# Kernel optimization log

Measured on AMD Instinct MI355X. Metric: run time of the kernel, lower is better.

Reference implementation:

```python
import jax, jax.numpy as jnp
import numpy as np

BITS = 4
GROUP = 128
MAXQ = 2 ** BITS - 1  # 15 for asymmetric 4-bit


def round_ste(x):
    # straight-through rounding: round in fwd, identity in bwd
    return x + jax.lax.stop_gradient(jnp.round(x) - x)


def quant_weight(weight, v, min_scale, max_scale):
    """Groupwise asymmetric fake-quant (quantize + dequantize) of weight.

    weight: [O, I], v: [O, I] learnable rounding offsets,
    min_scale/max_scale: [O*I/GROUP] learnable min/max scales in [-1, 0].
    """
    O, I = weight.shape
    w = weight.reshape(-1, GROUP)          # [G, GROUP]
    vv = v.reshape(-1, GROUP)              # [G, GROUP]
    wmin_t = jnp.minimum(w.min(axis=1), 0.0)  # [G]
    wmax_t = jnp.maximum(w.max(axis=1), 0.0)  # [G]
    # forward clamps min/max scale into [-1, 0] before use
    wmin = wmin_t * (jnp.clip(min_scale, -1.0, 0.0) + 1.0)
    wmax = wmax_t * (jnp.clip(max_scale, -1.0, 0.0) + 1.0)
    degenerate = (wmin == 0.0) & (wmax == 0.0)
    wmin = jnp.where(degenerate, -1.0, wmin)
    wmax = jnp.where(degenerate, 1.0, wmax)
    # scale stored at fp16 precision (scale_dtype), then used in fp32 math
    scale = ((wmax - wmin) / MAXQ).astype(jnp.float16).astype(weight.dtype)  # [G]
    zp = round_ste(-wmin / scale)                                            # [G]
    int_w = round_ste(w / scale[:, None] + vv)                               # [G, GROUP]
    q = jnp.clip(int_w + zp[:, None], 0.0, float(MAXQ))
    wq = scale[:, None] * (q - zp[:, None])
    return wq.reshape(O, I)


def setup_inputs() -> dict:
    key = jax.random.key(0)
    k_x, k_w, k_b, k_v = jax.random.split(key, 4)
    O, I = 4096, 4096
    B, S = 2, 2048
    x = jax.random.normal(k_x, (B, S, I), dtype=jnp.float32)
    weight = jax.random.normal(k_w, (O, I), dtype=jnp.float32) * 0.02
    bias = jax.random.normal(k_b, (O,), dtype=jnp.float32) * 0.02
    value = jax.random.normal(k_v, (O, I), dtype=jnp.float32) * 0.1
    n_groups = O * I // GROUP
    min_scale = jnp.zeros((n_groups,), dtype=jnp.float32)
    max_scale = jnp.zeros((n_groups,), dtype=jnp.float32)
    return {"x": x, "weight": weight, "bias": bias, "value": value,
            "min_scale": min_scale, "max_scale": max_scale}


def reference(x, weight, bias, value, min_scale, max_scale):
    wq = quant_weight(weight, value, min_scale, max_scale)  # [O, I]
    # F.linear(x, weight_q, bias): x @ wq.T + bias
    return jnp.einsum('bsi,oi->bso', x, wq) + bias
```

## Files before the change

### kernel.cpp

```cpp
#include <hip/hip_runtime.h>
#include <hip/hip_bf16.h>
#include <hip/hip_fp16.h>
#include <stdint.h>

#define M_DIM 4096
#define N_DIM 4096
#define K_DIM 4096
#define GROUPSZ 128
#define MAXQ 15.0f

#define BM 256
#define BN 256
#define BK 64
#define T_TILES (K_DIM / BK)

typedef __attribute__((ext_vector_type(8))) short short8;
typedef __attribute__((ext_vector_type(4))) float f32x4;

__global__ __launch_bounds__(256) void quant_kernel(
    const float* __restrict__ weight, const float* __restrict__ value,
    const float* __restrict__ min_scale, const float* __restrict__ max_scale,
    __hip_bfloat16* __restrict__ wq)
{
    const int tid  = threadIdx.x;
    const int wave = tid >> 6;
    const int lane = tid & 63;
    const long g    = (long)blockIdx.x * 4 + wave;
    const long base = g * GROUPSZ + lane * 2;

    const float2 w = *(const float2*)(weight + base);
    const float2 v = *(const float2*)(value  + base);

    float mn = fminf(w.x, w.y);
    float mx = fmaxf(w.x, w.y);
#pragma unroll
    for (int off = 32; off >= 1; off >>= 1) {
        mn = fminf(mn, __shfl_xor(mn, off, 64));
        mx = fmaxf(mx, __shfl_xor(mx, off, 64));
    }
    mn = fminf(mn, 0.0f);
    mx = fmaxf(mx, 0.0f);

    const float ms = fminf(fmaxf(min_scale[g], -1.0f), 0.0f) + 1.0f;
    const float xs = fminf(fmaxf(max_scale[g], -1.0f), 0.0f) + 1.0f;
    float wmin = mn * ms;
    float wmax = mx * xs;
    if (wmin == 0.0f && wmax == 0.0f) { wmin = -1.0f; wmax = 1.0f; }

    const float scale = (float)(_Float16)((wmax - wmin) / MAXQ);
    const float zp    = rintf(-wmin / scale);

    const float q0 = fminf(fmaxf(rintf(w.x / scale + v.x) + zp, 0.0f), MAXQ);
    const float q1 = fminf(fmaxf(rintf(w.y / scale + v.y) + zp, 0.0f), MAXQ);
    const float o0 = scale * (q0 - zp);
    const float o1 = scale * (q1 - zp);

    __hip_bfloat162 o;
    o.x = __float2bfloat16(o0);
    o.y = __float2bfloat16(o1);
    *(__hip_bfloat162*)(wq + base) = o;
}

__global__ __launch_bounds__(256) void cast_kernel(
    const float* __restrict__ x, __hip_bfloat16* __restrict__ xb)
{
    const long i = ((long)blockIdx.x * 256 + threadIdx.x) * 8;
    const float4 a = *(const float4*)(x + i);
    const float4 b = *(const float4*)(x + i + 4);
    union { short8 s; __hip_bfloat16 h[8]; } u;
    u.h[0] = __float2bfloat16(a.x);
    u.h[1] = __float2bfloat16(a.y);
    u.h[2] = __float2bfloat16(a.z);
    u.h[3] = __float2bfloat16(a.w);
    u.h[4] = __float2bfloat16(b.x);
    u.h[5] = __float2bfloat16(b.y);
    u.h[6] = __float2bfloat16(b.z);
    u.h[7] = __float2bfloat16(b.w);
    *(short8*)(xb + i) = u.s;
}

__global__ __launch_bounds__(512, 2) void gemm_kernel(
    const __hip_bfloat16* __restrict__ A,
    const __hip_bfloat16* __restrict__ B,
    const float* __restrict__ bias,
    float* __restrict__ C)
{
    __shared__ __align__(16) char lds[131072];

    const int tid  = threadIdx.x;
    const int lane = tid & 63;
    const int wv   = tid >> 6;
    const int wm   = wv >> 2;
    const int wn   = wv & 3;

    const int bid = blockIdx.x;
    const int swz = (bid & 7) * (gridDim.x >> 3) + (bid >> 3);
    const int brow = (swz >> 4) * BM;
    const int bcol = (swz & 15) * BN;

    const int stg_r = tid >> 3;
    const int cc    = ((tid & 7) ^ (stg_r & 7)) * 8;

#define STAGE(XP, rowbase, h, tau, ldsbase)                                         \
    { _Pragma("unroll")                                                             \
      for (int inst = 0; inst < 2; ++inst) {                                        \
        const __hip_bfloat16* g = (XP) +                                            \
            (size_t)((rowbase) + (h) * 128 + inst * 64 + stg_r) * K_DIM +           \
            (tau) * 64 + cc;                                                        \
        __builtin_amdgcn_global_load_lds(                                           \
            (const __attribute__((address_space(1))) void*)g,                       \
            (__attribute__((address_space(3))) void*)(lds + (ldsbase) +             \
                (h) * 16384 + inst * 8192 + (wv << 10)),                            \
            16, 0, 0);                                                              \
      } }

#define STAGE_TILE(tau, bc)                                                         \
    STAGE(A, brow, 0, tau, (bc) * 32768);                                           \
    STAGE(A, brow, 1, tau, (bc) * 32768);                                           \
    STAGE(B, bcol, 0, tau, 65536 + (bc) * 32768);                                   \
    STAGE(B, bcol, 1, tau, 65536 + (bc) * 32768);

    const int ro = lane & 15;
    const int hi = lane >> 4;
    const int slot0 = ((0 + hi) ^ (ro & 7)) << 4;
    const int slot1 = ((4 + hi) ^ (ro & 7)) << 4;
    const int rbA = (wm * 128 + ro) * 128;
    const int rbB = (wn * 64  + ro) * 128;

    f32x4 acc[8][4] = {};

#define MFMA_C(M0, AF, BF)                                                          \
    { _Pragma("unroll")                                                             \
      for (int n = 0; n < 4; ++n) {                                                 \
        _Pragma("unroll")                                                           \
        for (int mm = 0; mm < 4; ++mm)                                              \
            acc[(M0) + mm][n] = __builtin_amdgcn_mfma_f32_16x16x32_bf16(            \
                AF[mm], BF[n], acc[(M0) + mm][n], 0, 0, 0);                         \
      } }

#define RDA4(dst, base, M0, S)                                                      \
    dst[0] = *(const short8*)((base) + ((M0) + 0) * 2048 + (S));                    \
    dst[1] = *(const short8*)((base) + ((M0) + 1) * 2048 + (S));                    \
    dst[2] = *(const short8*)((base) + ((M0) + 2) * 2048 + (S));                    \
    dst[3] = *(const short8*)((base) + ((M0) + 3) * 2048 + (S));

#define RDB4(dst, base, S)                                                          \
    dst[0] = *(const short8*)((base) + 0 * 2048 + (S));                             \
    dst[1] = *(const short8*)((base) + 1 * 2048 + (S));                             \
    dst[2] = *(const short8*)((base) + 2 * 2048 + (S));                             \
    dst[3] = *(const short8*)((base) + 3 * 2048 + (S));

    short8 bfr0[4], bfr1[4];
    short8 afA[4], afB[4], afC[4], afD[4];

    STAGE_TILE(0, 0);
    asm volatile("s_waitcnt vmcnt(0)" ::: "memory");
    __builtin_amdgcn_s_barrier();
    RDA4(afA, lds + rbA, 0, slot0);
    RDB4(bfr0, lds + 65536 + rbB, slot0);

#pragma unroll 1
    for (int t = 0; t < T_TILES; ++t) {
        const int c = t & 1;
        const char* bA  = lds + c * 32768 + rbA;
        const char* bB  = lds + 65536 + c * 32768 + rbB;
        const char* bAn = lds + (c ^ 1) * 32768 + rbA;
        const char* bBn = lds + 65536 + (c ^ 1) * 32768 + rbB;

        if (t + 1 < T_TILES) { STAGE_TILE(t + 1, c ^ 1); }

        RDA4(afB, bA, 4, slot0);
        RDB4(bfr1, bB, slot1);
        asm volatile("s_waitcnt lgkmcnt(8)" ::: "memory");
        __builtin_amdgcn_sched_barrier(0);
        __builtin_amdgcn_s_setprio(1);
        MFMA_C(0, afA, bfr0);
        __builtin_amdgcn_s_setprio(0);

        RDA4(afC, bA, 0, slot1);
        asm volatile("s_waitcnt lgkmcnt(8)" ::: "memory");
        __builtin_amdgcn_sched_barrier(0);
        __builtin_amdgcn_s_setprio(1);
        MFMA_C(4, afB, bfr0);
        __builtin_amdgcn_s_setprio(0);

        RDA4(afD, bA, 4, slot1);
        asm volatile("s_waitcnt lgkmcnt(4)" ::: "memory");
        __builtin_amdgcn_sched_barrier(0);
        __builtin_amdgcn_s_setprio(1);
        MFMA_C(0, afC, bfr1);
        __builtin_amdgcn_s_setprio(0);

        asm volatile("s_waitcnt lgkmcnt(0)" ::: "memory");
        __builtin_amdgcn_sched_barrier(0);

        if (t + 1 < T_TILES) {
            asm volatile("s_waitcnt vmcnt(0)" ::: "memory");
            __builtin_amdgcn_s_barrier();
            RDA4(afA, bAn, 0, slot0);
            RDB4(bfr0, bBn, slot0);
            __builtin_amdgcn_sched_barrier(0);
        }

        __builtin_amdgcn_s_setprio(1);
        MFMA_C(4, afD, bfr1);
        __builtin_amdgcn_s_setprio(0);
    }

    const int col   = lane & 15;
    const int rbase = hi * 4;
    float bv[4];
#pragma unroll
    for (int n = 0; n < 4; ++n)
        bv[n] = bias[bcol + wn * 64 + n * 16 + col];

#pragma unroll
    for (int m = 0; m < 8; ++m) {
        const int mrow = brow + wm * 128 + m * 16 + rbase;
#pragma unroll
        for (int r = 0; r < 4; ++r) {
            float* crow = C + (size_t)(mrow + r) * N_DIM + bcol + wn * 64 + col;
#pragma unroll
            for (int n = 0; n < 4; ++n)
                crow[n * 16] = acc[m][n][r] + bv[n];
        }
    }
#undef STAGE
#undef STAGE_TILE
#undef MFMA_C
#undef RDA4
#undef RDB4
}

extern "C" void kernel_launch(void* const* d_in, const int* in_sizes, int n_in,
                              void* d_out, int out_size, void* d_ws, size_t ws_size,
                              hipStream_t stream) {
    const float* x         = (const float*)d_in[0];
    const float* weight    = (const float*)d_in[1];
    const float* bias      = (const float*)d_in[2];
    const float* value     = (const float*)d_in[3];
    const float* min_scale = (const float*)d_in[4];
    const float* max_scale = (const float*)d_in[5];
    float* out = (float*)d_out;

    __hip_bfloat16* xb  = (__hip_bfloat16*)d_ws;
    __hip_bfloat16* wqb = xb + (size_t)M_DIM * K_DIM;

    quant_kernel<<<(N_DIM * K_DIM / GROUPSZ) / 4, 256, 0, stream>>>(
        weight, value, min_scale, max_scale, wqb);
    cast_kernel<<<(M_DIM * K_DIM) / (256 * 8), 256, 0, stream>>>(x, xb);
    gemm_kernel<<<(M_DIM / BM) * (N_DIM / BN), 512, 0, stream>>>(xb, wqb, bias, out);
}
```

Baseline: 167.9 us.

## Switch GEMM inner loop from 16x16x32 to 32x32x16 bf16 MFMA

Replaces the 16x16x32 bf16 MFMA tiling with 32x32x16 MFMA instructions. Each wave now holds a 4x2 grid of 32x32 accumulators, and the LDS fragment loads are reorganised into four K-slices with a new XOR swizzle. The epilogue is rewritten for the 32x32 output layout. The larger MFMA is meant to halve the number of LDS fragment reads per FLOP and the instruction issue count, at the cost of a different bank-access pattern and a more scattered output store.

```diff
diff --git a/kernel.cpp b/kernel.cpp
--- a/kernel.cpp
+++ b/kernel.cpp
@@ -15,7 +15,7 @@
 #define T_TILES (K_DIM / BK)
 
 typedef __attribute__((ext_vector_type(8))) short short8;
-typedef __attribute__((ext_vector_type(4))) float f32x4;
+typedef __attribute__((ext_vector_type(16))) float f32x16;
 
 __global__ __launch_bounds__(256) void quant_kernel(
     const float* __restrict__ weight, const float* __restrict__ value,
@@ -120,44 +120,45 @@
     STAGE(B, bcol, 0, tau, 65536 + (bc) * 32768);                                   \
     STAGE(B, bcol, 1, tau, 65536 + (bc) * 32768);
 
-    const int ro = lane & 15;
-    const int hi = lane >> 4;
-    const int slot0 = ((0 + hi) ^ (ro & 7)) << 4;
-    const int slot1 = ((4 + hi) ^ (ro & 7)) << 4;
-    const int rbA = (wm * 128 + ro) * 128;
-    const int rbB = (wn * 64  + ro) * 128;
-
-    f32x4 acc[8][4] = {};
-
-#define MFMA_C(M0, AF, BF)                                                          \
+    const int ro32 = lane & 31;
+    const int hi2  = lane >> 5;
+    const int sw   = ro32 & 7;
+    const int sk0 = ((0 + hi2) ^ sw) << 4;
+    const int sk1 = ((2 + hi2) ^ sw) << 4;
+    const int sk2 = ((4 + hi2) ^ sw) << 4;
+    const int sk3 = ((6 + hi2) ^ sw) << 4;
+    const int rbA = (wm * 128 + ro32) * 128;
+    const int rbB = (wn * 64  + ro32) * 128;
+
+    f32x16 acc[4][2] = {};
+
+#define MFMA8(AF, BF)                                                               \
     { _Pragma("unroll")                                                             \
-      for (int n = 0; n < 4; ++n) {                                                 \
+      for (int nb = 0; nb < 2; ++nb) {                                              \
         _Pragma("unroll")                                                           \
-        for (int mm = 0; mm < 4; ++mm)                                              \
-            acc[(M0) + mm][n] = __builtin_amdgcn_mfma_f32_16x16x32_bf16(            \
-                AF[mm], BF[n], acc[(M0) + mm][n], 0, 0, 0);                         \
+        for (int mb = 0; mb < 4; ++mb)                                              \
+            acc[mb][nb] = __builtin_amdgcn_mfma_f32_32x32x16_bf16(                  \
+                AF[mb], BF[nb], acc[mb][nb], 0, 0, 0);                              \
       } }
 
-#define RDA4(dst, base, M0, S)                                                      \
-    dst[0] = *(const short8*)((base) + ((M0) + 0) * 2048 + (S));                    \
-    dst[1] = *(const short8*)((base) + ((M0) + 1) * 2048 + (S));                    \
-    dst[2] = *(const short8*)((base) + ((M0) + 2) * 2048 + (S));                    \
-    dst[3] = *(const short8*)((base) + ((M0) + 3) * 2048 + (S));
-
-#define RDB4(dst, base, S)                                                          \
-    dst[0] = *(const short8*)((base) + 0 * 2048 + (S));                             \
-    dst[1] = *(const short8*)((base) + 1 * 2048 + (S));                             \
-    dst[2] = *(const short8*)((base) + 2 * 2048 + (S));                             \
-    dst[3] = *(const short8*)((base) + 3 * 2048 + (S));
-
-    short8 bfr0[4], bfr1[4];
-    short8 afA[4], afB[4], afC[4], afD[4];
+#define RDA(dst, base, SK)                                                          \
+    dst[0] = *(const short8*)((base) + 0 * 4096 + (SK));                            \
+    dst[1] = *(const short8*)((base) + 1 * 4096 + (SK));                            \
+    dst[2] = *(const short8*)((base) + 2 * 4096 + (SK));                            \
+    dst[3] = *(const short8*)((base) + 3 * 4096 + (SK));
+
+#define RDB(dst, base, SK)                                                          \
+    dst[0] = *(const short8*)((base) + 0 * 4096 + (SK));                            \
+    dst[1] = *(const short8*)((base) + 1 * 4096 + (SK));
+
+    short8 afE[4], bfE[2];
+    short8 afO[4], bfO[2];
 
     STAGE_TILE(0, 0);
     asm volatile("s_waitcnt vmcnt(0)" ::: "memory");
     __builtin_amdgcn_s_barrier();
-    RDA4(afA, lds + rbA, 0, slot0);
-    RDB4(bfr0, lds + 65536 + rbB, slot0);
+    RDA(afE, lds + rbA, sk0);
+    RDB(bfE, lds + 65536 + rbB, sk0);
 
 #pragma unroll 1
     for (int t = 0; t < T_TILES; ++t) {
@@ -169,67 +170,64 @@
 
         if (t + 1 < T_TILES) { STAGE_TILE(t + 1, c ^ 1); }
 
-        RDA4(afB, bA, 4, slot0);
-        RDB4(bfr1, bB, slot1);
-        asm volatile("s_waitcnt lgkmcnt(8)" ::: "memory");
-        __builtin_amdgcn_sched_barrier(0);
-        __builtin_amdgcn_s_setprio(1);
-        MFMA_C(0, afA, bfr0);
-        __builtin_amdgcn_s_setprio(0);
-
-        RDA4(afC, bA, 0, slot1);
-        asm volatile("s_waitcnt lgkmcnt(8)" ::: "memory");
-        __builtin_amdgcn_sched_barrier(0);
-        __builtin_amdgcn_s_setprio(1);
-        MFMA_C(4, afB, bfr0);
-        __builtin_amdgcn_s_setprio(0);
-
-        RDA4(afD, bA, 4, slot1);
-        asm volatile("s_waitcnt lgkmcnt(4)" ::: "memory");
-        __builtin_amdgcn_sched_barrier(0);
-        __builtin_amdgcn_s_setprio(1);
-        MFMA_C(0, afC, bfr1);
+        RDA(afO, bA, sk1); RDB(bfO, bB, sk1);
+        asm volatile("s_waitcnt lgkmcnt(6)" ::: "memory");
+        __builtin_amdgcn_sched_barrier(0);
+        __builtin_amdgcn_s_setprio(1);
+        MFMA8(afE, bfE);
+        __builtin_amdgcn_s_setprio(0);
+
+        RDA(afE, bA, sk2); RDB(bfE, bB, sk2);
+        asm volatile("s_waitcnt lgkmcnt(6)" ::: "memory");
+        __builtin_amdgcn_sched_barrier(0);
+        __builtin_amdgcn_s_setprio(1);
+        MFMA8(afO, bfO);
+        __builtin_amdgcn_s_setprio(0);
+
+        RDA(afO, bA, sk3); RDB(bfO, bB, sk3);
+        asm volatile("s_waitcnt lgkmcnt(6)" ::: "memory");
+        __builtin_amdgcn_sched_barrier(0);
+        __builtin_amdgcn_s_setprio(1);
+        MFMA8(afE, bfE);
         __builtin_amdgcn_s_setprio(0);
 
         asm volatile("s_waitcnt lgkmcnt(0)" ::: "memory");
         __builtin_amdgcn_sched_barrier(0);
-
         if (t + 1 < T_TILES) {
             asm volatile("s_waitcnt vmcnt(0)" ::: "memory");
             __builtin_amdgcn_s_barrier();
-            RDA4(afA, bAn, 0, slot0);
-            RDB4(bfr0, bBn, slot0);
+            RDA(afE, bAn, sk0);
+            RDB(bfE, bBn, sk0);
             __builtin_amdgcn_sched_barrier(0);
         }
 
         __builtin_amdgcn_s_setprio(1);
-        MFMA_C(4, afD, bfr1);
+        MFMA8(afO, bfO);
         __builtin_amdgcn_s_setprio(0);
     }
 
-    const int col   = lane & 15;
-    const int rbase = hi * 4;
-    float bv[4];
-#pragma unroll
-    for (int n = 0; n < 4; ++n)
-        bv[n] = bias[bcol + wn * 64 + n * 16 + col];
-
-#pragma unroll
-    for (int m = 0; m < 8; ++m) {
-        const int mrow = brow + wm * 128 + m * 16 + rbase;
-#pragma unroll
-        for (int r = 0; r < 4; ++r) {
-            float* crow = C + (size_t)(mrow + r) * N_DIM + bcol + wn * 64 + col;
-#pragma unroll
-            for (int n = 0; n < 4; ++n)
-                crow[n * 16] = acc[m][n][r] + bv[n];
+    float bv[2];
+#pragma unroll
+    for (int nb = 0; nb < 2; ++nb)
+        bv[nb] = bias[bcol + wn * 64 + nb * 32 + ro32];
+
+#pragma unroll
+    for (int mb = 0; mb < 4; ++mb) {
+#pragma unroll
+        for (int nb = 0; nb < 2; ++nb) {
+#pragma unroll
+            for (int i = 0; i < 16; ++i) {
+                const int row = brow + wm * 128 + mb * 32 + (i & 3) + ((i >> 2) * 8) + hi2 * 4;
+                C[(size_t)row * N_DIM + bcol + wn * 64 + nb * 32 + ro32] =
+                    acc[mb][nb][i] + bv[nb];
+            }
         }
     }
 #undef STAGE
 #undef STAGE_TILE
-#undef MFMA_C
-#undef RDA4
-#undef RDB4
+#undef MFMA8
+#undef RDA
+#undef RDB
 }
 
 extern "C" void kernel_launch(void* const* d_in, const int* in_sizes, int n_in,
```

After: 184.3 us. 1.1x slower.

## Merge quant and cast kernels; interleave B-tile prefetch between MFMA clusters

Applied to the files above, without the earlier changes.

The weight-quant and activation-cast kernels become one launch, with the block index choosing which job each block does. This removes one launch and the gap between the two kernels. In the GEMM main loop, the global-to-LDS prefetch of the B tile is split so that its two halves are issued between MFMA clusters instead of all at once at the top. The aim is to spread memory issue across the compute phase, at the risk of scheduler interactions with the lgkmcnt waits.

```diff
diff --git a/kernel.cpp b/kernel.cpp
--- a/kernel.cpp
+++ b/kernel.cpp
@@ -14,69 +14,72 @@
 #define BK 64
 #define T_TILES (K_DIM / BK)
 
+#define QUANT_BLOCKS (N_DIM * K_DIM / GROUPSZ / 4)
+#define CAST_BLOCKS  (M_DIM * K_DIM / (256 * 8))
+
 typedef __attribute__((ext_vector_type(8))) short short8;
 typedef __attribute__((ext_vector_type(4))) float f32x4;
 
-__global__ __launch_bounds__(256) void quant_kernel(
+__global__ __launch_bounds__(256) void prep_kernel(
     const float* __restrict__ weight, const float* __restrict__ value,
     const float* __restrict__ min_scale, const float* __restrict__ max_scale,
-    __hip_bfloat16* __restrict__ wq)
-{
-    const int tid  = threadIdx.x;
-    const int wave = tid >> 6;
-    const int lane = tid & 63;
-    const long g    = (long)blockIdx.x * 4 + wave;
-    const long base = g * GROUPSZ + lane * 2;
-
-    const float2 w = *(const float2*)(weight + base);
-    const float2 v = *(const float2*)(value  + base);
-
-    float mn = fminf(w.x, w.y);
-    float mx = fmaxf(w.x, w.y);
-#pragma unroll
-    for (int off = 32; off >= 1; off >>= 1) {
-        mn = fminf(mn, __shfl_xor(mn, off, 64));
-        mx = fmaxf(mx, __shfl_xor(mx, off, 64));
-    }
-    mn = fminf(mn, 0.0f);
-    mx = fmaxf(mx, 0.0f);
-
-    const float ms = fminf(fmaxf(min_scale[g], -1.0f), 0.0f) + 1.0f;
-    const float xs = fminf(fmaxf(max_scale[g], -1.0f), 0.0f) + 1.0f;
-    float wmin = mn * ms;
-    float wmax = mx * xs;
-    if (wmin == 0.0f && wmax == 0.0f) { wmin = -1.0f; wmax = 1.0f; }
-
-    const float scale = (float)(_Float16)((wmax - wmin) / MAXQ);
-    const float zp    = rintf(-wmin / scale);
-
-    const float q0 = fminf(fmaxf(rintf(w.x / scale + v.x) + zp, 0.0f), MAXQ);
-    const float q1 = fminf(fmaxf(rintf(w.y / scale + v.y) + zp, 0.0f), MAXQ);
-    const float o0 = scale * (q0 - zp);
-    const float o1 = scale * (q1 - zp);
-
-    __hip_bfloat162 o;
-    o.x = __float2bfloat16(o0);
-    o.y = __float2bfloat16(o1);
-    *(__hip_bfloat162*)(wq + base) = o;
-}
-
-__global__ __launch_bounds__(256) void cast_kernel(
+    __hip_bfloat16* __restrict__ wq,
     const float* __restrict__ x, __hip_bfloat16* __restrict__ xb)
 {
-    const long i = ((long)blockIdx.x * 256 + threadIdx.x) * 8;
-    const float4 a = *(const float4*)(x + i);
-    const float4 b = *(const float4*)(x + i + 4);
-    union { short8 s; __hip_bfloat16 h[8]; } u;
-    u.h[0] = __float2bfloat16(a.x);
-    u.h[1] = __float2bfloat16(a.y);
-    u.h[2] = __float2bfloat16(a.z);
-    u.h[3] = __float2bfloat16(a.w);
-    u.h[4] = __float2bfloat16(b.x);
-    u.h[5] = __float2bfloat16(b.y);
-    u.h[6] = __float2bfloat16(b.z);
-    u.h[7] = __float2bfloat16(b.w);
-    *(short8*)(xb + i) = u.s;
+    const int bidx = blockIdx.x;
+    const int tid  = threadIdx.x;
+    if (bidx < QUANT_BLOCKS) {
+        const int wave = tid >> 6;
+        const int lane = tid & 63;
+        const long g    = (long)bidx * 4 + wave;
+        const long base = g * GROUPSZ + lane * 2;
+
+        const float2 w = *(const float2*)(weight + base);
+        const float2 v = *(const float2*)(value  + base);
+
+        float mn = fminf(w.x, w.y);
+        float mx = fmaxf(w.x, w.y);
+#pragma unroll
+        for (int off = 32; off >= 1; off >>= 1) {
+            mn = fminf(mn, __shfl_xor(mn, off, 64));
+            mx = fmaxf(mx, __shfl_xor(mx, off, 64));
+        }
+        mn = fminf(mn, 0.0f);
+        mx = fmaxf(mx, 0.0f);
+
+        const float ms = fminf(fmaxf(min_scale[g], -1.0f), 0.0f) + 1.0f;
+        const float xs = fminf(fmaxf(max_scale[g], -1.0f), 0.0f) + 1.0f;
+        float wmin = mn * ms;
+        float wmax = mx * xs;
+        if (wmin == 0.0f && wmax == 0.0f) { wmin = -1.0f; wmax = 1.0f; }
+
+        const float scale = (float)(_Float16)((wmax - wmin) / MAXQ);
+        const float zp    = rintf(-wmin / scale);
+
+        const float q0 = fminf(fmaxf(rintf(w.x / scale + v.x) + zp, 0.0f), MAXQ);
+        const float q1 = fminf(fmaxf(rintf(w.y / scale + v.y) + zp, 0.0f), MAXQ);
+        const float o0 = scale * (q0 - zp);
+        const float o1 = scale * (q1 - zp);
+
+        __hip_bfloat162 o;
+        o.x = __float2bfloat16(o0);
+        o.y = __float2bfloat16(o1);
+        *(__hip_bfloat162*)(wq + base) = o;
+    } else {
+        const long i = ((long)(bidx - QUANT_BLOCKS) * 256 + tid) * 8;
+        const float4 a = *(const float4*)(x + i);
+        const float4 b = *(const float4*)(x + i + 4);
+        union { short8 s; __hip_bfloat16 h[8]; } u;
+        u.h[0] = __float2bfloat16(a.x);
+        u.h[1] = __float2bfloat16(a.y);
+        u.h[2] = __float2bfloat16(a.z);
+        u.h[3] = __float2bfloat16(a.w);
+        u.h[4] = __float2bfloat16(b.x);
+        u.h[5] = __float2bfloat16(b.y);
+        u.h[6] = __float2bfloat16(b.z);
+        u.h[7] = __float2bfloat16(b.w);
+        *(short8*)(xb + i) = u.s;
+    }
 }
 
 __global__ __launch_bounds__(512, 2) void gemm_kernel(
@@ -114,12 +117,6 @@
             16, 0, 0);                                                              \
       } }
 
-#define STAGE_TILE(tau, bc)                                                         \
-    STAGE(A, brow, 0, tau, (bc) * 32768);                                           \
-    STAGE(A, brow, 1, tau, (bc) * 32768);                                           \
-    STAGE(B, bcol, 0, tau, 65536 + (bc) * 32768);                                   \
-    STAGE(B, bcol, 1, tau, 65536 + (bc) * 32768);
-
     const int ro = lane & 15;
     const int hi = lane >> 4;
     const int slot0 = ((0 + hi) ^ (ro & 7)) << 4;
@@ -153,7 +150,10 @@
     short8 bfr0[4], bfr1[4];
     short8 afA[4], afB[4], afC[4], afD[4];
 
-    STAGE_TILE(0, 0);
+    STAGE(A, brow, 0, 0, 0);
+    STAGE(A, brow, 1, 0, 0);
+    STAGE(B, bcol, 0, 0, 65536);
+    STAGE(B, bcol, 1, 0, 65536);
     asm volatile("s_waitcnt vmcnt(0)" ::: "memory");
     __builtin_amdgcn_s_barrier();
     RDA4(afA, lds + rbA, 0, slot0);
@@ -167,7 +167,10 @@
         const char* bAn = lds + (c ^ 1) * 32768 + rbA;
         const char* bBn = lds + 65536 + (c ^ 1) * 32768 + rbB;
 
-        if (t + 1 < T_TILES) { STAGE_TILE(t + 1, c ^ 1); }
+        if (t + 1 < T_TILES) {
+            STAGE(A, brow, 0, t + 1, (c ^ 1) * 32768);
+            STAGE(A, brow, 1, t + 1, (c ^ 1) * 32768);
+        }
 
         RDA4(afB, bA, 4, slot0);
         RDB4(bfr1, bB, slot1);
@@ -176,6 +179,7 @@
         __builtin_amdgcn_s_setprio(1);
         MFMA_C(0, afA, bfr0);
         __builtin_amdgcn_s_setprio(0);
+        if (t + 1 < T_TILES) { STAGE(B, bcol, 0, t + 1, 65536 + (c ^ 1) * 32768); }
 
         RDA4(afC, bA, 0, slot1);
         asm volatile("s_waitcnt lgkmcnt(8)" ::: "memory");
@@ -183,6 +187,7 @@
         __builtin_amdgcn_s_setprio(1);
         MFMA_C(4, afB, bfr0);
         __builtin_amdgcn_s_setprio(0);
+        if (t + 1 < T_TILES) { STAGE(B, bcol, 1, t + 1, 65536 + (c ^ 1) * 32768); }
 
         RDA4(afD, bA, 4, slot1);
         asm volatile("s_waitcnt lgkmcnt(4)" ::: "memory");
@@ -226,7 +231,6 @@
         }
     }
 #undef STAGE
-#undef STAGE_TILE
 #undef MFMA_C
 #undef RDA4
 #undef RDB4
@@ -246,8 +250,7 @@
     __hip_bfloat16* xb  = (__hip_bfloat16*)d_ws;
     __hip_bfloat16* wqb = xb + (size_t)M_DIM * K_DIM;
 
-    quant_kernel<<<(N_DIM * K_DIM / GROUPSZ) / 4, 256, 0, stream>>>(
-        weight, value, min_scale, max_scale, wqb);
-    cast_kernel<<<(M_DIM * K_DIM) / (256 * 8), 256, 0, stream>>>(x, xb);
+    prep_kernel<<<QUANT_BLOCKS + CAST_BLOCKS, 256, 0, stream>>>(
+        weight, value, min_scale, max_scale, wqb, x, xb);
     gemm_kernel<<<(M_DIM / BM) * (N_DIM / BN), 512, 0, stream>>>(xb, wqb, bias, out);
 }
```

Measured after the change: 166.4 us, median of 3. About the same (-0.9%).
